# Optimization experiments

Measured on AMD Instinct MI355X. Metric: run time of the kernel, lower is better.

The kernel has to match this reference:

```python
import jax, jax.numpy as jnp
import numpy as np

N = 262144   # tokens
L = 128      # ldims (per-direction LSTM feature size)
H = 128      # hidden_units
H2 = 128     # hidden2_units
R = 64       # number of relation labels


def setup_inputs() -> dict:
    key = jax.random.key(0)
    ks = jax.random.split(key, 12)
    glorot = lambda k, shape: jax.random.uniform(
        k, shape, jnp.float32, -1.0, 1.0) * np.sqrt(6.0 / (shape[0] + shape[1]))
    return {
        "fwd": jax.random.normal(ks[0], (N, L), jnp.float32),
        "bwd": jax.random.normal(ks[1], (N, L), jnp.float32),
        "gold_heads": jax.random.randint(ks[2], (N - 1,), 0, N),
        "gold_rels": jax.random.randint(ks[3], (N - 1,), 0, R),
        "WFOH": glorot(ks[4], (2 * L, H)),
        "WFOM": glorot(ks[5], (2 * L, H)),
        "rhidBias": glorot(ks[6], (1, H)),
        "rcatBias": glorot(ks[7], (1, 2 * H)),
        "rhid2Layer": glorot(ks[8], (2 * H, H2)),
        "rhid2Bias": glorot(ks[9], (1, H2)),
        "routLayer": glorot(ks[10], (H2, R)),
        "routBias": glorot(ks[11], (1, R)),
    }


def reference(fwd, bwd, gold_heads, gold_rels, WFOH, WFOM, rhidBias,
              rcatBias, rhid2Layer, rhid2Bias, routLayer, routBias):
    E = gold_heads.shape[0]
    mods = jnp.arange(E) + 1                       # modifiers are tokens 1..N-1
    # per-edge concat(head fwd-state, modifier bwd-state): (E, 2L)
    cat = jnp.concatenate([fwd[gold_heads], bwd[mods]], axis=-1)
    headfov = cat @ WFOH                           # (E, H)
    modfov = cat @ WFOM                            # (E, H)
    # hidden2_units > 0 branch of __evaluateLabel
    h = jnp.tanh(jnp.concatenate([headfov, modfov], axis=-1) + rcatBias)  # (E, 2H)
    h2 = jnp.tanh(h @ rhid2Layer + rhid2Bias)      # (E, H2)
    scores = h2 @ routLayer + routBias             # (E, R)
    # hinge: best wrong label vs gold label, loss only if margin violated
    gold_s = jnp.take_along_axis(scores, gold_rels[:, None], axis=1)[:, 0]
    masked = jnp.where(jnp.arange(R)[None, :] == gold_rels[:, None], -jnp.inf, scores)
    wrong_idx = jnp.argmax(masked, axis=1)
    wrong_s = jnp.take_along_axis(scores, wrong_idx[:, None], axis=1)[:, 0]
    lerrs = jnp.where(gold_s < wrong_s + 1.0, wrong_s - gold_s, 0.0)  # (E,)
    return lerrs
```

## Files before the change

### kernel.cpp

```cpp
#include <hip/hip_runtime.h>
#include <hip/hip_bf16.h>

typedef __bf16 bf16x8 __attribute__((ext_vector_type(8)));
typedef float  f32x4  __attribute__((ext_vector_type(4)));

#define MFMA16 __builtin_amdgcn_mfma_f32_16x16x32_bf16

__device__ __forceinline__ float fast_tanh(float x) {
    float e = __builtin_amdgcn_exp2f(x * 2.8853900817779268f);
    return 1.0f - 2.0f * __builtin_amdgcn_rcpf(e + 1.0f);
}

__device__ __forceinline__ int kinv(int ke) {
    return (ke & ~31) | ((ke & 1) << 4) | ((ke >> 1) & 15);
}

__device__ __forceinline__ bf16x8 cvt2(const float4 a, const float4 b) {
    bf16x8 t;
    t[0] = (__bf16)a.x; t[1] = (__bf16)a.y; t[2] = (__bf16)a.z; t[3] = (__bf16)a.w;
    t[4] = (__bf16)b.x; t[5] = (__bf16)b.y; t[6] = (__bf16)b.z; t[7] = (__bf16)b.w;
    return t;
}

__global__ __launch_bounds__(256) void preconv_kernel(
    const float* __restrict__ WFOH, const float* __restrict__ WFOM,
    const float* __restrict__ rhid2Layer, const float* __restrict__ routLayer,
    char* __restrict__ ws)
{
    const int f = blockIdx.x * 256 + threadIdx.x;
    bf16x8 v;
    char* dst;
    if (f < 8192) {
        const int lane = f & 63, t = f >> 6;
        const int nbl = t & 1, kk = (t >> 1) & 7, w = t >> 4;
        const int g = lane >> 4, c = lane & 15;
        const int nb = 32 * w + 16 * nbl;
        const float* Wsrc = (nb < 128) ? WFOH : WFOM;
        const int col = (nb + c) & 127;
        #pragma unroll
        for (int j = 0; j < 8; ++j) v[j] = (__bf16)Wsrc[(32 * kk + 8 * g + j) * 128 + col];
        dst = ws + (size_t)f * 16;
    } else if (f < 12288) {
        const int f2 = f - 8192;
        const int lane = f2 & 63, t = f2 >> 6;
        const int nbl = t & 1, kk = (t >> 1) & 7, q4 = t >> 4;
        const int g = lane >> 4, c = lane & 15;
        const int n2 = 32 * q4 + 16 * nbl + c;
        #pragma unroll
        for (int j = 0; j < 8; ++j) v[j] = (__bf16)rhid2Layer[kinv(32 * kk + 8 * g + j) * 128 + n2];
        dst = ws + 131072 + (size_t)f2 * 16;
    } else if (f < 13312) {
        const int f3 = f - 12288;
        const int lane = f3 & 63, t = f3 >> 6;
        const int kk = t & 3, q4 = t >> 2;
        const int g = lane >> 4, c = lane & 15;
        const int n3 = 16 * q4 + c;
        #pragma unroll
        for (int j = 0; j < 8; ++j) v[j] = (__bf16)routLayer[kinv(32 * kk + 8 * g + j) * 64 + n3];
        dst = ws + 196608 + (size_t)f3 * 16;
    } else {
        return;
    }
    *(bf16x8*)dst = v;
}

template<bool PRE>
__device__ __forceinline__ bf16x8 wfrag1(const char* ws, const float* WFOH, const float* WFOM,
                                         int w, int kk, int nbl, int lane) {
    if constexpr (PRE) {
        return *(const bf16x8*)(ws + (size_t)w * 16384 + kk * 2048 + nbl * 1024 + lane * 16);
    } else {
        const int g = lane >> 4, c = lane & 15;
        const int nb = 32 * w + 16 * nbl;
        const float* Wsrc = (nb < 128) ? WFOH : WFOM;
        const int col = (nb + c) & 127;
        bf16x8 v;
        #pragma unroll
        for (int j = 0; j < 8; ++j) v[j] = (__bf16)Wsrc[(32 * kk + 8 * g + j) * 128 + col];
        return v;
    }
}
template<bool PRE>
__device__ __forceinline__ bf16x8 wfrag2(const char* ws, const float* rhid2Layer,
                                         int q4, int kk, int nbl, int lane) {
    if constexpr (PRE) {
        return *(const bf16x8*)(ws + 131072 + (size_t)q4 * 16384 + kk * 2048 + nbl * 1024 + lane * 16);
    } else {
        const int g = lane >> 4, c = lane & 15;
        const int n2 = 32 * q4 + 16 * nbl + c;
        bf16x8 v;
        #pragma unroll
        for (int j = 0; j < 8; ++j) v[j] = (__bf16)rhid2Layer[kinv(32 * kk + 8 * g + j) * 128 + n2];
        return v;
    }
}
template<bool PRE>
__device__ __forceinline__ bf16x8 wfrag3(const char* ws, const float* routLayer,
                                         int nb, int kk, int lane) {
    if constexpr (PRE) {
        return *(const bf16x8*)(ws + 196608 + (size_t)nb * 4096 + kk * 1024 + lane * 16);
    } else {
        const int g = lane >> 4, c = lane & 15;
        const int n3 = 16 * nb + c;
        bf16x8 v;
        #pragma unroll
        for (int j = 0; j < 8; ++j) v[j] = (__bf16)routLayer[kinv(32 * kk + 8 * g + j) * 64 + n3];
        return v;
    }
}

template<bool PRE>
__global__ __launch_bounds__(512, 2) void rel_kernel(
    const float* __restrict__ fwd, const float* __restrict__ bwd,
    const int* __restrict__ gold_heads, const int* __restrict__ gold_rels,
    const float* __restrict__ WFOH, const float* __restrict__ WFOM,
    const float* __restrict__ rcatBias, const float* __restrict__ rhid2Layer,
    const float* __restrict__ rhid2Bias, const float* __restrict__ routLayer,
    const float* __restrict__ routBias, const char* __restrict__ wstab,
    int* __restrict__ fixcnt, int* __restrict__ fixlist, int fixcap,
    float* __restrict__ out, int E, int NT)
{
    __shared__ __align__(16) char smem[81920];
    char* const sh_cat = smem;
    char* const sh_h   = smem + 32768;
    char* const sh_h2  = smem + 65536;

    const int tid   = threadIdx.x;
    const int w     = tid >> 6;
    const int lane  = tid & 63;
    const int row16 = lane & 15;
    const int g     = lane >> 4;
    const int xm    = (row16 & 7) << 4;

    const int r_s = tid >> 3;
    const int q_s = tid & 7;
    const int xr  = (r_s & 7) << 4;

    const float rcb0 = rcatBias[32 * w + row16];
    const float rcb1 = rcatBias[32 * w + 16 + row16];
    const float r2b  = rhid2Bias[16 * w + row16];
    float rob[4];
    #pragma unroll
    for (int nb = 0; nb < 4; ++nb) rob[nb] = routBias[16 * nb + row16];

    bf16x8 pfb[4];
    {
        const int e = blockIdx.x * 64 + r_s;
        int nh0 = 0;
        if (q_s < 4 && e < E) nh0 = gold_heads[e];
        if (e < E) {
            const float* src = (q_s < 4) ? (fwd + (size_t)nh0 * 128 + 32 * q_s)
                                         : (bwd + (size_t)(e + 1) * 128 + 32 * (q_s - 4));
            const float4* p4 = (const float4*)src;
            #pragma unroll
            for (int i = 0; i < 4; ++i) pfb[i] = cvt2(p4[2 * i], p4[2 * i + 1]);
        } else {
            #pragma unroll
            for (int i = 0; i < 4; ++i) pfb[i] = cvt2(make_float4(0.f,0.f,0.f,0.f), make_float4(0.f,0.f,0.f,0.f));
        }
    }

    for (int tile = blockIdx.x; tile < NT; tile += gridDim.x) {
        const int e0 = tile * 64;
        const int tnext = tile + gridDim.x;
        const bool hn = tnext < NT;

        int zoff = 0;
        asm volatile("" : "+v"(zoff));
        const char*  wsL  = wstab + zoff;
        const float* W1aL = WFOH + zoff;
        const float* W1bL = WFOM + zoff;
        const float* W2L  = rhid2Layer + zoff;
        const float* W3L  = routLayer + zoff;

        int nh = 0; bool gv = false;
        if (hn) {
            const int en = tnext * 64 + r_s;
            gv = en < E;
            if (q_s < 4 && gv) nh = gold_heads[en];
        }

        #pragma unroll
        for (int i = 0; i < 4; ++i)
            *(bf16x8*)(sh_cat + r_s * 512 + ((64 * q_s + 16 * i) ^ xr)) = pfb[i];

        int gr[4] = {0, 0, 0, 0};
        if (w < 4) {
            #pragma unroll
            for (int i = 0; i < 4; ++i) {
                const int e = e0 + 16 * w + 4 * g + i;
                if (e < E) gr[i] = gold_rels[e];
            }
        }
        __syncthreads();

        float4 pfA[8];
        if (hn && gv) {
            const float4* p4 = (const float4*)((q_s < 4)
                                 ? (fwd + (size_t)nh * 128 + 32 * q_s)
                                 : (bwd + (size_t)(tnext * 64 + r_s + 1) * 128 + 32 * (q_s - 4)));
            #pragma unroll
            for (int i = 0; i < 8; ++i) pfA[i] = p4[i];
        } else {
            #pragma unroll
            for (int i = 0; i < 8; ++i) pfA[i] = make_float4(0.f, 0.f, 0.f, 0.f);
        }

        f32x4 acc1[4][2];
        #pragma unroll
        for (int i = 0; i < 4; ++i) {
            acc1[i][0] = (f32x4){0.f, 0.f, 0.f, 0.f};
            acc1[i][1] = (f32x4){0.f, 0.f, 0.f, 0.f};
        }
        #pragma unroll
        for (int kk = 0; kk < 8; ++kk) {
            const bf16x8 b0 = wfrag1<PRE>(wsL, W1aL, W1bL, w, kk, 0, lane);
            const bf16x8 b1 = wfrag1<PRE>(wsL, W1aL, W1bL, w, kk, 1, lane);
            const int ko = (64 * kk + 16 * g) ^ xm;
            #pragma unroll
            for (int mb = 0; mb < 4; ++mb) {
                const bf16x8 a = *(const bf16x8*)(sh_cat + (16 * mb + row16) * 512 + ko);
                acc1[mb][0] = MFMA16(a, b0, acc1[mb][0], 0, 0, 0);
                acc1[mb][1] = MFMA16(a, b1, acc1[mb][1], 0, 0, 0);
            }
        }
        #pragma unroll
        for (int mb = 0; mb < 4; ++mb) {
            #pragma unroll
            for (int r = 0; r < 4; ++r) {
                const int row = 16 * mb + 4 * g + r;
                const __bf16 p0 = (__bf16)fast_tanh(acc1[mb][0][r] + rcb0);
                const __bf16 p1 = (__bf16)fast_tanh(acc1[mb][1][r] + rcb1);
                const unsigned u = (unsigned)__builtin_bit_cast(unsigned short, p0)
                                 | ((unsigned)__builtin_bit_cast(unsigned short, p1) << 16);
                *(unsigned*)(sh_h + row * 512 + ((64 * w + 4 * row16) ^ ((row & 7) << 4))) = u;
            }
        }
        __syncthreads();

        f32x4 acc2[4];
        #pragma unroll
        for (int i = 0; i < 4; ++i) acc2[i] = (f32x4){0.f, 0.f, 0.f, 0.f};
        #pragma unroll
        for (int kk = 0; kk < 8; ++kk) {
            const bf16x8 b2 = wfrag2<PRE>(wsL, W2L, w >> 1, kk, w & 1, lane);
            const int ko = (64 * kk + 16 * g) ^ xm;
            #pragma unroll
            for (int mb = 0; mb < 4; ++mb) {
                const bf16x8 a = *(const bf16x8*)(sh_h + (16 * mb + row16) * 512 + ko);
                acc2[mb] = MFMA16(a, b2, acc2[mb], 0, 0, 0);
            }
        }
        #pragma unroll
        for (int mb = 0; mb < 4; ++mb) {
            #pragma unroll
            for (int r = 0; r < 4; ++r) {
                const int row = 16 * mb + 4 * g + r;
                const __bf16 p = (__bf16)fast_tanh(acc2[mb][r] + r2b);
                *(unsigned short*)(sh_h2 + row * 256 +
                    ((64 * (w >> 1) + 4 * row16 + 2 * (w & 1)) ^ ((row & 7) << 4)))
                    = __builtin_bit_cast(unsigned short, p);
            }
        }
        #pragma unroll
        for (int i = 0; i < 4; ++i) pfb[i] = cvt2(pfA[2 * i], pfA[2 * i + 1]);
        __syncthreads();

        if (w < 4) {
            bf16x8 a3[4];
            #pragma unroll
            for (int kk = 0; kk < 4; ++kk)
                a3[kk] = *(const bf16x8*)(sh_h2 + (16 * w + row16) * 256 + ((64 * kk + 16 * g) ^ xm));
            f32x4 acc3[4];
            #pragma unroll
            for (int nb = 0; nb < 4; ++nb) {
                acc3[nb] = (f32x4){0.f, 0.f, 0.f, 0.f};
                #pragma unroll
                for (int kk = 0; kk < 4; ++kk) {
                    const bf16x8 b = wfrag3<PRE>(wsL, W3L, nb, kk, lane);
                    acc3[nb] = MFMA16(a3[kk], b, acc3[nb], 0, 0, 0);
                }
            }
            #pragma unroll
            for (int i = 0; i < 4; ++i) {
                const int gold = gr[i];
                float gs = -3.0e38f, ws_ = -3.0e38f;
                #pragma unroll
                for (int nb = 0; nb < 4; ++nb) {
                    const float v = acc3[nb][i] + rob[nb];
                    const int lab = 16 * nb + row16;
                    if (lab == gold) gs = v; else ws_ = fmaxf(ws_, v);
                }
                gs = fmaxf(gs, __shfl_xor(gs, 1)); ws_ = fmaxf(ws_, __shfl_xor(ws_, 1));
                gs = fmaxf(gs, __shfl_xor(gs, 2)); ws_ = fmaxf(ws_, __shfl_xor(ws_, 2));
                gs = fmaxf(gs, __shfl_xor(gs, 4)); ws_ = fmaxf(ws_, __shfl_xor(ws_, 4));
                gs = fmaxf(gs, __shfl_xor(gs, 8)); ws_ = fmaxf(ws_, __shfl_xor(ws_, 8));
                const int e = e0 + 16 * w + 4 * g + i;
                if (row16 == 0 && e < E) {
                    out[e] = (gs < ws_ + 1.0f) ? (ws_ - gs) : 0.0f;
                    if (fabsf((gs - ws_) - 1.0f) < 0.125f && fixcap > 0) {
                        const int idx = atomicAdd(fixcnt, 1);
                        if (idx < fixcap) fixlist[idx] = e;
                    }
                }
            }
        }
    }
}

__global__ __launch_bounds__(256) void fixup_kernel(
    const float* __restrict__ fwd, const float* __restrict__ bwd,
    const int* __restrict__ gold_heads, const int* __restrict__ gold_rels,
    const float* __restrict__ WFOH, const float* __restrict__ WFOM,
    const float* __restrict__ rcatBias, const float* __restrict__ rhid2Layer,
    const float* __restrict__ rhid2Bias, const float* __restrict__ routLayer,
    const float* __restrict__ routBias,
    const int* __restrict__ fixcnt, const int* __restrict__ fixlist, int fixcap,
    float* __restrict__ out)
{
    __shared__ float fx_cat[256];
    __shared__ float fx_h[256];
    __shared__ float fx_h2[128];
    __shared__ float fx_p[256];
    int n = *fixcnt;
    if (n > fixcap) n = fixcap;
    const int tid = threadIdx.x;
    for (int i = blockIdx.x; i < n; i += gridDim.x) {
        const int e = fixlist[i];
        {
            const int head = gold_heads[e];
            fx_cat[tid] = (tid < 128) ? fwd[(size_t)head * 128 + tid]
                                      : bwd[(size_t)(e + 1) * 128 + (tid - 128)];
        }
        __syncthreads();
        {
            const float* base = (tid < 128) ? WFOH : WFOM;
            const int col = tid & 127;
            float s = 0.f;
            #pragma unroll 8
            for (int k = 0; k < 256; ++k) s += fx_cat[k] * base[k * 128 + col];
            fx_h[tid] = tanhf(s + rcatBias[tid]);
        }
        __syncthreads();
        {
            const int d = tid & 127, hh = tid >> 7;
            float s = 0.f;
            #pragma unroll 8
            for (int k = 128 * hh; k < 128 * hh + 128; ++k) s += fx_h[k] * rhid2Layer[k * 128 + d];
            fx_p[hh * 128 + d] = s;
        }
        __syncthreads();
        if (tid < 128) fx_h2[tid] = tanhf(fx_p[tid] + fx_p[128 + tid] + rhid2Bias[tid]);
        __syncthreads();
        {
            const int d = tid & 63, qq = tid >> 6;
            float s = 0.f;
            #pragma unroll 8
            for (int k = 32 * qq; k < 32 * qq + 32; ++k) s += fx_h2[k] * routLayer[k * 64 + d];
            fx_p[qq * 64 + d] = s;
        }
        __syncthreads();
        if (tid < 64) {
            const float v = fx_p[tid] + fx_p[64 + tid] + fx_p[128 + tid] + fx_p[192 + tid] + routBias[tid];
            const int gold = gold_rels[e];
            float gs = (tid == gold) ? v : -3.0e38f;
            float wv = (tid == gold) ? -3.0e38f : v;
            #pragma unroll
            for (int o = 1; o < 64; o <<= 1) {
                gs = fmaxf(gs, __shfl_xor(gs, o));
                wv = fmaxf(wv, __shfl_xor(wv, o));
            }
            if (tid == 0) out[e] = (gs < wv + 1.0f) ? (wv - gs) : 0.0f;
        }
        __syncthreads();
    }
}

extern "C" void kernel_launch(void* const* d_in, const int* in_sizes, int n_in,
                              void* d_out, int out_size, void* d_ws, size_t ws_size,
                              hipStream_t stream) {
    const float* fwd        = (const float*)d_in[0];
    const float* bwd        = (const float*)d_in[1];
    const int*   gold_heads = (const int*)d_in[2];
    const int*   gold_rels  = (const int*)d_in[3];
    const float* WFOH       = (const float*)d_in[4];
    const float* WFOM       = (const float*)d_in[5];
    const float* rcatBias   = (const float*)d_in[7];
    const float* rhid2      = (const float*)d_in[8];
    const float* rhid2Bias  = (const float*)d_in[9];
    const float* rout       = (const float*)d_in[10];
    const float* routBias   = (const float*)d_in[11];
    float* out = (float*)d_out;

    const int E = in_sizes[2];
    if (E <= 0) return;
    const int NT = (E + 63) / 64;
    const int grid = NT < 512 ? NT : 512;

    const size_t TAB = 212992;
    const int FIXCAP = 8192;
    const size_t FIX_BYTES = 4 + 4 * (size_t)FIXCAP;

    const bool pre = ws_size >= TAB + FIX_BYTES;
    int* fixcnt = nullptr;
    int* fixlist = nullptr;
    int fixcap = 0;
    if (pre) {
        fixcnt = (int*)((char*)d_ws + TAB);
        fixlist = fixcnt + 1;
        fixcap = FIXCAP;
    } else if (ws_size >= FIX_BYTES) {
        fixcnt = (int*)d_ws;
        fixlist = fixcnt + 1;
        fixcap = FIXCAP;
    }
    if (fixcap) hipMemsetAsync(fixcnt, 0, 4, stream);

    if (pre) {
        hipLaunchKernelGGL(preconv_kernel, dim3(52), dim3(256), 0, stream,
                           WFOH, WFOM, rhid2, rout, (char*)d_ws);
        hipLaunchKernelGGL((rel_kernel<true>), dim3(grid), dim3(512), 0, stream,
                           fwd, bwd, gold_heads, gold_rels, WFOH, WFOM, rcatBias,
                           rhid2, rhid2Bias, rout, routBias, (const char*)d_ws,
                           fixcnt, fixlist, fixcap, out, E, NT);
    } else {
        hipLaunchKernelGGL((rel_kernel<false>), dim3(grid), dim3(512), 0, stream,
                           fwd, bwd, gold_heads, gold_rels, WFOH, WFOM, rcatBias,
                           rhid2, rhid2Bias, rout, routBias, (const char*)nullptr,
                           fixcnt, fixlist, fixcap, out, E, NT);
    }
    if (fixcap) {
        hipLaunchKernelGGL(fixup_kernel, dim3(120), dim3(256), 0, stream,
                           fwd, bwd, gold_heads, gold_rels, WFOH, WFOM, rcatBias,
                           rhid2, rhid2Bias, rout, routBias,
                           fixcnt, fixlist, fixcap, out);
    }
}
```

Before: 185.4 us.

## Double-buffer LDS tiles with rotated swizzle and raise MFMA wave priority

Cuts shared memory from 80KB to 64KB by ping-ponging two 32KB regions between the concat/h2 buffers and the hidden buffer across tiles. The XOR swizzle is replaced by a rotation-based 16-byte chunk layout, which changes the k-permutation so the layer-3 weight no longer needs kinv. s_setprio is raised around the MFMA loops. Lower LDS per block could allow more resident blocks, and the new layout aims to reduce bank conflicts. The risk is that the buffer aliasing across tiles is correct only if the sync points suffice.

```diff
diff --git a/kernel.cpp b/kernel.cpp
--- a/kernel.cpp
+++ b/kernel.cpp
@@ -52,11 +52,11 @@
     } else if (f < 13312) {
         const int f3 = f - 12288;
         const int lane = f3 & 63, t = f3 >> 6;
-        const int kk = t & 3, q4 = t >> 2;
-        const int g = lane >> 4, c = lane & 15;
-        const int n3 = 16 * q4 + c;
-        #pragma unroll
-        for (int j = 0; j < 8; ++j) v[j] = (__bf16)routLayer[kinv(32 * kk + 8 * g + j) * 64 + n3];
+        const int kk = t & 3, nb = t >> 2;
+        const int g = lane >> 4, c = lane & 15;
+        const int n3 = 16 * nb + c;
+        #pragma unroll
+        for (int j = 0; j < 8; ++j) v[j] = (__bf16)routLayer[(32 * kk + 8 * g + j) * 64 + n3];
         dst = ws + 196608 + (size_t)f3 * 16;
     } else {
         return;
@@ -104,7 +104,7 @@
         const int n3 = 16 * nb + c;
         bf16x8 v;
         #pragma unroll
-        for (int j = 0; j < 8; ++j) v[j] = (__bf16)routLayer[kinv(32 * kk + 8 * g + j) * 64 + n3];
+        for (int j = 0; j < 8; ++j) v[j] = (__bf16)routLayer[(32 * kk + 8 * g + j) * 64 + n3];
         return v;
     }
 }
@@ -120,21 +120,16 @@
     int* __restrict__ fixcnt, int* __restrict__ fixlist, int fixcap,
     float* __restrict__ out, int E, int NT)
 {
-    __shared__ __align__(16) char smem[81920];
-    char* const sh_cat = smem;
-    char* const sh_h   = smem + 32768;
-    char* const sh_h2  = smem + 65536;
+    __shared__ __align__(16) char smem[65536];
 
     const int tid   = threadIdx.x;
     const int w     = tid >> 6;
     const int lane  = tid & 63;
     const int row16 = lane & 15;
     const int g     = lane >> 4;
-    const int xm    = (row16 & 7) << 4;
 
     const int r_s = tid >> 3;
     const int q_s = tid & 7;
-    const int xr  = (r_s & 7) << 4;
 
     const float rcb0 = rcatBias[32 * w + row16];
     const float rcb1 = rcatBias[32 * w + 16 + row16];
@@ -160,7 +155,12 @@
         }
     }
 
-    for (int tile = blockIdx.x; tile < NT; tile += gridDim.x) {
+    int pp = 0;
+    for (int tile = blockIdx.x; tile < NT; tile += gridDim.x, pp ^= 1) {
+        char* const sh_cat = smem + (pp ? 32768 : 0);
+        char* const sh_h   = smem + (pp ? 0 : 32768);
+        char* const sh_h2  = sh_cat;
+
         const int e0 = tile * 64;
         const int tnext = tile + gridDim.x;
         const bool hn = tnext < NT;
@@ -182,7 +182,7 @@
 
         #pragma unroll
         for (int i = 0; i < 4; ++i)
-            *(bf16x8*)(sh_cat + r_s * 512 + ((64 * q_s + 16 * i) ^ xr)) = pfb[i];
+            *(bf16x8*)(sh_cat + r_s * 512 + 16 * ((4 * q_s + i + r_s) & 31)) = pfb[i];
 
         int gr[4] = {0, 0, 0, 0};
         if (w < 4) {
@@ -212,18 +212,20 @@
             acc1[i][0] = (f32x4){0.f, 0.f, 0.f, 0.f};
             acc1[i][1] = (f32x4){0.f, 0.f, 0.f, 0.f};
         }
+        __builtin_amdgcn_s_setprio(1);
         #pragma unroll
         for (int kk = 0; kk < 8; ++kk) {
             const bf16x8 b0 = wfrag1<PRE>(wsL, W1aL, W1bL, w, kk, 0, lane);
             const bf16x8 b1 = wfrag1<PRE>(wsL, W1aL, W1bL, w, kk, 1, lane);
-            const int ko = (64 * kk + 16 * g) ^ xm;
             #pragma unroll
             for (int mb = 0; mb < 4; ++mb) {
-                const bf16x8 a = *(const bf16x8*)(sh_cat + (16 * mb + row16) * 512 + ko);
+                const int R = 16 * mb + row16;
+                const bf16x8 a = *(const bf16x8*)(sh_cat + R * 512 + 16 * ((4 * kk + g + R) & 31));
                 acc1[mb][0] = MFMA16(a, b0, acc1[mb][0], 0, 0, 0);
                 acc1[mb][1] = MFMA16(a, b1, acc1[mb][1], 0, 0, 0);
             }
         }
+        __builtin_amdgcn_s_setprio(0);
         #pragma unroll
         for (int mb = 0; mb < 4; ++mb) {
             #pragma unroll
@@ -231,9 +233,10 @@
                 const int row = 16 * mb + 4 * g + r;
                 const __bf16 p0 = (__bf16)fast_tanh(acc1[mb][0][r] + rcb0);
                 const __bf16 p1 = (__bf16)fast_tanh(acc1[mb][1][r] + rcb1);
-                const unsigned u = (unsigned)__builtin_bit_cast(unsigned short, p0)
-                                 | ((unsigned)__builtin_bit_cast(unsigned short, p1) << 16);
-                *(unsigned*)(sh_h + row * 512 + ((64 * w + 4 * row16) ^ ((row & 7) << 4))) = u;
+                const unsigned uval = (unsigned)__builtin_bit_cast(unsigned short, p0)
+                                    | ((unsigned)__builtin_bit_cast(unsigned short, p1) << 16);
+                const int u = 4 * w + (row16 >> 2);
+                *(unsigned*)(sh_h + row * 512 + 16 * ((u + row) & 31) + 4 * (row16 & 3)) = uval;
             }
         }
         __syncthreads();
@@ -241,24 +244,26 @@
         f32x4 acc2[4];
         #pragma unroll
         for (int i = 0; i < 4; ++i) acc2[i] = (f32x4){0.f, 0.f, 0.f, 0.f};
+        __builtin_amdgcn_s_setprio(1);
         #pragma unroll
         for (int kk = 0; kk < 8; ++kk) {
             const bf16x8 b2 = wfrag2<PRE>(wsL, W2L, w >> 1, kk, w & 1, lane);
-            const int ko = (64 * kk + 16 * g) ^ xm;
             #pragma unroll
             for (int mb = 0; mb < 4; ++mb) {
-                const bf16x8 a = *(const bf16x8*)(sh_h + (16 * mb + row16) * 512 + ko);
+                const int R = 16 * mb + row16;
+                const bf16x8 a = *(const bf16x8*)(sh_h + R * 512 + 16 * ((4 * kk + g + R) & 31));
                 acc2[mb] = MFMA16(a, b2, acc2[mb], 0, 0, 0);
             }
         }
+        __builtin_amdgcn_s_setprio(0);
         #pragma unroll
         for (int mb = 0; mb < 4; ++mb) {
             #pragma unroll
             for (int r = 0; r < 4; ++r) {
                 const int row = 16 * mb + 4 * g + r;
                 const __bf16 p = (__bf16)fast_tanh(acc2[mb][r] + r2b);
-                *(unsigned short*)(sh_h2 + row * 256 +
-                    ((64 * (w >> 1) + 4 * row16 + 2 * (w & 1)) ^ ((row & 7) << 4)))
+                const int u2 = 2 * w + (row16 >> 3);
+                *(unsigned short*)(sh_h2 + row * 256 + 16 * ((u2 + row) & 15) + 2 * (row16 & 7))
                     = __builtin_bit_cast(unsigned short, p);
             }
         }
@@ -269,9 +274,12 @@
         if (w < 4) {
             bf16x8 a3[4];
             #pragma unroll
-            for (int kk = 0; kk < 4; ++kk)
-                a3[kk] = *(const bf16x8*)(sh_h2 + (16 * w + row16) * 256 + ((64 * kk + 16 * g) ^ xm));
+            for (int kk = 0; kk < 4; ++kk) {
+                const int R3 = 16 * w + row16;
+                a3[kk] = *(const bf16x8*)(sh_h2 + R3 * 256 + 16 * ((4 * kk + g + R3) & 15));
+            }
             f32x4 acc3[4];
+            __builtin_amdgcn_s_setprio(1);
             #pragma unroll
             for (int nb = 0; nb < 4; ++nb) {
                 acc3[nb] = (f32x4){0.f, 0.f, 0.f, 0.f};
@@ -281,6 +289,7 @@
                     acc3[nb] = MFMA16(a3[kk], b, acc3[nb], 0, 0, 0);
                 }
             }
+            __builtin_amdgcn_s_setprio(0);
             #pragma unroll
             for (int i = 0; i < 4; ++i) {
                 const int gold = gr[i];
```

Measured after the change: 176.9 us. 4.5% less time.
